# Kernel optimization log

Measured on AMD Instinct MI355X. Metric: run time of the kernel, lower is better.

The kernel has to match this reference:

```python
import jax, jax.numpy as jnp
import numpy as np
import math

MAX_LEN = 65536
NUM_HEADS = 16
HEAD_DIM = 64
K_MAX = 64
LOCAL_WINDOW = 512
LOG_N = math.ceil(math.log2(MAX_LEN + 1))   # 17
LEAF_START = 2 ** LOG_N                      # segment-tree leaf offset


def cover_set(pos):
    """O(log n) segment-tree nodes covering prefix [0..pos-1], each with leaf-depth."""
    if pos <= 0:
        return []
    l, r = LEAF_START, LEAF_START + min(pos, MAX_LEN)
    out = []
    while l < r:
        if l & 1:
            out.append((l, LOG_N - int(math.floor(math.log2(l)))))
            l += 1
        if r & 1:
            r -= 1
            out.append((r, LOG_N - int(math.floor(math.log2(r)))))
        l >>= 1
        r >>= 1
    return out


def node_content(v_tokens, node_idx, depth):
    """Content of a FULL subtree node under the concat/pairwise-mean gated merge.
    Equals: concat tokens while K<=k_max, then (left+right)/2 elementwise, which
    collapses to a strided mean over chunks of size L//K_MAX. Returns (H, K, D)."""
    L = 1 << depth
    a = (node_idx << depth) - LEAF_START          # first token covered by node
    chunk = v_tokens[a:a + L]                     # (L, H, D), static slice
    if L <= K_MAX:
        f = chunk                                 # (L, H, D)
    else:
        f = chunk.reshape(L // K_MAX, K_MAX, NUM_HEADS, HEAD_DIM).mean(0)  # (K_MAX,H,D)
    return jnp.transpose(f, (1, 0, 2))            # (H, K, D)


def setup_inputs() -> dict:
    key = jax.random.key(0)
    k1, k2, k3 = jax.random.split(key, 3)
    v_tokens = jax.random.normal(k1, (50000, NUM_HEADS, HEAD_DIM), jnp.float32)
    q_new = jax.random.normal(k2, (1, NUM_HEADS, HEAD_DIM), jnp.float32)
    depth_proj_w = jax.random.normal(k3, (LOG_N + 1, HEAD_DIM, HEAD_DIM), jnp.float32) * 0.02
    depth_temp = jnp.linspace(0.5, 4.0, LOG_N + 1).astype(jnp.float32)
    return {"v_tokens": v_tokens, "q_new": q_new, "depth_proj_w": depth_proj_w,
            "depth_temp": depth_temp, "n_tokens": 50000}


def reference(v_tokens, q_new, depth_proj_w, depth_temp, n_tokens):
    pos = int(n_tokens)
    q = q_new[0]                                   # (H, D)
    inv_sqrt_d = 1.0 / math.sqrt(HEAD_DIM)

    # --- local window attention over last min(pos, W) tokens (chronological) ---
    n_local = min(pos, LOCAL_WINDOW)
    v_local = v_tokens[pos - n_local:pos]          # (W, H, D)
    s = jnp.einsum('hd,khd->hk', q, v_local) * inv_sqrt_d
    w = jax.nn.softmax(s, axis=-1)
    local_out = jnp.einsum('hk,khd->hd', w, v_local)   # (H, D)

    # --- multi-depth causal tree attention over the O(log n) cover set ---
    node_outs = []
    for node_idx, depth in cover_set(pos):
        f = node_content(v_tokens, node_idx, depth)    # (H, K, D)
        q_depth = q + q @ depth_proj_w[depth].T        # depth-specific query delta
        scale = 1.0 / ((jax.nn.softplus(depth_temp[depth]) + 1e-6) * math.sqrt(HEAD_DIM))
        s = jnp.einsum('hd,hkd->hk', q_depth, f) * scale
        w = jnp.einsum('hk,hkd->hd', jax.nn.softmax(s, axis=-1), f)
        node_outs.append(w)
    if node_outs:
        tree_out = jnp.stack(node_outs, axis=0).mean(0)
    else:
        tree_out = jnp.zeros_like(local_out)

    return (local_out + tree_out)[None]            # (1, H, D)
```

## Files before the change

kernel.cpp:

```cpp
#include <hip/hip_runtime.h>
#include <math.h>

#define NUM_HEADS   16
#define HEAD_DIM    64
#define KMAXN       64
#define LOCAL_WIN   512
#define LOG_N       17
#define LEAF_START  131072
#define MAX_LEN_TOK 65536
#define ROW         1024
#define SLICE       65536
#define MAXN        34

typedef float vf4 __attribute__((ext_vector_type(4)));

__device__ __forceinline__ vf4 ntload(const float* p) {
    return __builtin_nontemporal_load((const vf4*)p);
}

struct K1Args {
    int nNodes;
    int a[MAXN];
    int cpb[MAXN];
    int C[MAXN];
    int CB[MAXN];
    int K[MAXN];
    int off[MAXN];
    int bbase[MAXN];
};

struct K2Args {
    int nNodes;
    int K[MAXN];
    int C[MAXN];
    int CB[MAXN];
    int off[MAXN];
    int a[MAXN];
    int depth[MAXN];
};

__global__ __launch_bounds__(256, 4) void k1_reduce(const float* __restrict__ v,
                                                    float* __restrict__ ws,
                                                    K1Args A) {
    int b = blockIdx.x;
    int node = 0;
    for (int i = 1; i < A.nNodes; ++i)
        if (b >= A.bbase[i]) node = i;
    int lb  = b - A.bbase[node];
    int K   = A.K[node];
    int kgc = (K + 3) >> 2;
    int cb  = lb / kgc;
    int kg  = lb - cb * kgc;
    int k0  = kg * 4;
    int RK  = K - k0; if (RK > 4) RK = 4;
    int c0  = cb * A.cpb[node];
    int c1  = c0 + A.cpb[node];
    int C   = A.C[node];
    if (c1 > C) c1 = C;

    int j4 = threadIdx.x * 4;

    vf4 acc0 = 0.f, acc1 = 0.f, acc2 = 0.f, acc3 = 0.f;

    if (RK == 4) {
        int c = c0;
        for (; c + 2 <= c1; c += 2) {
            const float* p0 = v + (long)(A.a[node] + c * 64 + k0) * ROW + j4;
            const float* p1 = p0 + SLICE;
            vf4 y0 = ntload(p0);
            vf4 y1 = ntload(p0 + ROW);
            vf4 y2 = ntload(p0 + 2 * ROW);
            vf4 y3 = ntload(p0 + 3 * ROW);
            vf4 z0 = ntload(p1);
            vf4 z1 = ntload(p1 + ROW);
            vf4 z2 = ntload(p1 + 2 * ROW);
            vf4 z3 = ntload(p1 + 3 * ROW);
            acc0 += y0 + z0; acc1 += y1 + z1; acc2 += y2 + z2; acc3 += y3 + z3;
        }
        if (c < c1) {
            const float* p0 = v + (long)(A.a[node] + c * 64 + k0) * ROW + j4;
            acc0 += ntload(p0);
            acc1 += ntload(p0 + ROW);
            acc2 += ntload(p0 + 2 * ROW);
            acc3 += ntload(p0 + 3 * ROW);
        }
    } else {
        for (int c = c0; c < c1; ++c) {
            const float* p0 = v + (long)(A.a[node] + c * 64 + k0) * ROW + j4;
            if (RK > 0) acc0 += ntload(p0);
            if (RK > 1) acc1 += ntload(p0 + ROW);
            if (RK > 2) acc2 += ntload(p0 + 2 * ROW);
            if (RK > 3) acc3 += ntload(p0 + 3 * ROW);
        }
    }

    float* wp = ws + (long)A.off[node] + (long)cb * SLICE + (long)k0 * ROW + j4;
    if (RK > 0) *(vf4*)(wp)           = acc0;
    if (RK > 1) *(vf4*)(wp + ROW)     = acc1;
    if (RK > 2) *(vf4*)(wp + 2 * ROW) = acc2;
    if (RK > 3) *(vf4*)(wp + 3 * ROW) = acc3;
}

__global__ __launch_bounds__(512) void k2_fused(const float* __restrict__ v,
                                                const float* __restrict__ ws,
                                                const float* __restrict__ q,
                                                const float* __restrict__ W,
                                                const float* __restrict__ temp,
                                                float* __restrict__ node_out,
                                                float* __restrict__ local_out,
                                                int pos, K2Args A) {
    int h    = blockIdx.x;
    int node = blockIdx.y;
    int tid  = threadIdx.x;
    int lane = tid & 63;
    int w    = tid >> 6;

    __shared__ float fh[64][64];
    __shared__ float qs[64], qds[64], sv[64], ps[64];
    __shared__ float red[8][64];
    __shared__ float sc[LOCAL_WIN];
    __shared__ float wred[16];
    __shared__ float mS[2];

    if (node < A.nNodes) {
        int K = A.K[node];
        if (tid < 64) qs[tid] = q[h * 64 + tid];

        const float* bp; int CB; float invC;
        if (A.C[node] > 1) {
            bp   = ws + (long)A.off[node] + h * 64;
            CB   = A.CB[node];
            invC = 1.0f / (float)A.C[node];
        } else {
            bp   = v + (long)A.a[node] * ROW + h * 64;
            CB   = 1;
            invC = 1.0f;
        }
        for (int id = tid; id < 1024; id += 512) {
            int r  = id >> 4;
            int c4 = (id & 15) << 2;
            if (r < K) {
                vf4 s0 = 0.f, s1 = 0.f, s2 = 0.f, s3 = 0.f;
                const float* p = bp + (long)r * ROW + c4;
                int cb = 0;
                for (; cb + 4 <= CB; cb += 4) {
                    s0 += *(const vf4*)(p + (long)cb * SLICE);
                    s1 += *(const vf4*)(p + (long)(cb + 1) * SLICE);
                    s2 += *(const vf4*)(p + (long)(cb + 2) * SLICE);
                    s3 += *(const vf4*)(p + (long)(cb + 3) * SLICE);
                }
                for (; cb < CB; ++cb) s0 += *(const vf4*)(p + (long)cb * SLICE);
                s0 += s1; s2 += s3; s0 += s2;
                s0 *= invC;
                *(vf4*)&fh[r][c4] = s0;
            }
        }
        __syncthreads();

        int dep = A.depth[node];
        float qp = 0.f;
        const float* Wr = W + ((long)dep * 64 + lane) * 64;
        #pragma unroll
        for (int e = w * 8; e < w * 8 + 8; ++e) qp += qs[e] * Wr[e];
        red[w][lane] = qp;
        __syncthreads();
        if (w == 0) {
            float t = qs[lane];
            #pragma unroll
            for (int i = 0; i < 8; ++i) t += red[i][lane];
            qds[lane] = t;
        }
        __syncthreads();
        float qd    = qds[lane];
        float sp    = log1pf(expf(temp[dep]));
        float scale = 1.0f / ((sp + 1e-6f) * 8.0f);

        for (int k = w; k < K; k += 8) {
            float p = qd * fh[k][lane];
            #pragma unroll
            for (int m = 1; m < 64; m <<= 1) p += __shfl_xor(p, m, 64);
            if (lane == 0) sv[k] = p * scale;
        }
        __syncthreads();

        if (w == 0) {
            float s  = (lane < K) ? sv[lane] : -1e30f;
            float mx = s;
            #pragma unroll
            for (int m = 1; m < 64; m <<= 1) mx = fmaxf(mx, __shfl_xor(mx, m, 64));
            float e = (lane < K) ? expf(s - mx) : 0.f;
            float S = e;
            #pragma unroll
            for (int m = 1; m < 64; m <<= 1) S += __shfl_xor(S, m, 64);
            ps[lane] = e / S;
        }
        __syncthreads();

        float o = 0.f;
        for (int k = w; k < K; k += 8) o += ps[k] * fh[k][lane];
        red[w][lane] = o;
        __syncthreads();
        if (w == 0) {
            float t = 0.f;
            #pragma unroll
            for (int i = 0; i < 8; ++i) t += red[i][lane];
            node_out[node * ROW + h * 64 + lane] = t;
        }
    } else {
        int nloc = pos < LOCAL_WIN ? pos : LOCAL_WIN;
        int t0   = pos - nloc;

        if (tid < 64) qs[tid] = q[h * 64 + tid];
        __syncthreads();

        float s = -1e30f;
        if (tid < nloc) {
            const float* vr = v + (long)(t0 + tid) * ROW + h * 64;
            float acc = 0.f;
            #pragma unroll 8
            for (int d = 0; d < 64; ++d) acc += qs[d] * vr[d];
            s = acc * 0.125f;
        }
        float mx = s;
        #pragma unroll
        for (int m = 1; m < 64; m <<= 1) mx = fmaxf(mx, __shfl_xor(mx, m, 64));
        if (lane == 0) wred[w] = mx;
        __syncthreads();
        if (tid == 0) {
            float m2 = wred[0];
            for (int i = 1; i < 8; ++i) m2 = fmaxf(m2, wred[i]);
            mS[0] = m2;
        }
        __syncthreads();
        float m = mS[0];

        float e = (tid < nloc) ? expf(s - m) : 0.f;
        sc[tid] = e;
        float su = e;
        #pragma unroll
        for (int mm = 1; mm < 64; mm <<= 1) su += __shfl_xor(su, mm, 64);
        if (lane == 0) wred[8 + w] = su;
        __syncthreads();
        if (tid == 0) {
            float S2 = 0.f;
            for (int i = 0; i < 8; ++i) S2 += wred[8 + i];
            mS[1] = S2;
        }
        __syncthreads();
        float S = mS[1];

        float acc = 0.f;
        {
            const float* vb = v + (long)t0 * ROW + h * 64 + lane;
            int tb = w * 64;
            #pragma unroll 4
            for (int i = 0; i < 64; ++i) {
                int t = tb + i;
                if (t < nloc) acc += sc[t] * vb[(long)t * ROW];
            }
        }
        red[w][lane] = acc;
        __syncthreads();

        if (w == 0) {
            float tot = 0.f;
            #pragma unroll
            for (int i = 0; i < 8; ++i) tot += red[i][lane];
            local_out[h * 64 + lane] = (nloc > 0) ? tot / S : 0.f;
        }
    }
}

__global__ __launch_bounds__(256) void k3_combine(const float* __restrict__ node_out,
                                                  const float* __restrict__ local_out,
                                                  int nNodes,
                                                  float* __restrict__ out) {
    int i = blockIdx.x * 256 + threadIdx.x;
    float tr = 0.f;
    for (int n = 0; n < nNodes; ++n) tr += node_out[(long)n * ROW + i];
    if (nNodes > 0) tr /= (float)nNodes;
    out[i] = local_out[i] + tr;
}

static int floor_log2_host(unsigned x) { int r = 0; while (x >>= 1) ++r; return r; }

extern "C" void kernel_launch(void* const* d_in, const int* in_sizes, int n_in,
                              void* d_out, int out_size, void* d_ws, size_t ws_size,
                              hipStream_t stream) {
    const float* v    = (const float*)d_in[0];
    const float* q    = (const float*)d_in[1];
    const float* W    = (const float*)d_in[2];
    const float* temp = (const float*)d_in[3];
    float* out        = (float*)d_out;
    float* ws         = (float*)d_ws;

    int pos = in_sizes[0] / ROW;

    int n_nodes = 0;
    int nv[MAXN], nd[MAXN];
    if (pos > 0) {
        long l = LEAF_START;
        long r = LEAF_START + (pos < MAX_LEN_TOK ? pos : MAX_LEN_TOK);
        while (l < r) {
            if (l & 1) { nv[n_nodes] = (int)l; nd[n_nodes] = LOG_N - floor_log2_host((unsigned)l); ++n_nodes; ++l; }
            if (r & 1) { --r; nv[n_nodes] = (int)r; nd[n_nodes] = LOG_N - floor_log2_host((unsigned)r); ++n_nodes; }
            l >>= 1; r >>= 1;
        }
    }

    int cpb_choice = 1024;
    for (int cand : {16, 32, 64, 128, 256, 512, 1024}) {
        long tot_cb = 0;
        for (int i = 0; i < n_nodes; ++i) {
            int L = 1 << nd[i];
            int C = (L > KMAXN) ? L / KMAXN : 1;
            if (C > 1) tot_cb += (C + cand - 1) / cand;
        }
        long need = (tot_cb * (long)SLICE + (long)n_nodes * ROW + ROW) * 4;
        if (need <= (long)ws_size) { cpb_choice = cand; break; }
    }

    K1Args A1{}; K2Args A2{};
    A2.nNodes = n_nodes;
    int off = 0, bb = 0, nBig = 0;
    for (int i = 0; i < n_nodes; ++i) {
        int depth = nd[i];
        int L = 1 << depth;
        int a = (nv[i] << depth) - LEAF_START;
        int K = (L < KMAXN) ? L : KMAXN;
        int C = (L > KMAXN) ? L / KMAXN : 1;
        A2.K[i] = K; A2.C[i] = C; A2.a[i] = a; A2.depth[i] = depth;
        if (C > 1) {
            int CB  = (C + cpb_choice - 1) / cpb_choice;
            int cpb = (C + CB - 1) / CB;
            int kgc = (K + 3) / 4;
            A1.a[nBig] = a;   A1.cpb[nBig] = cpb; A1.C[nBig] = C;
            A1.CB[nBig] = CB; A1.K[nBig] = K;
            A1.off[nBig] = off; A1.bbase[nBig] = bb;
            A2.CB[i] = CB; A2.off[i] = off;
            off += CB * SLICE;
            bb  += kgc * CB;
            ++nBig;
        } else {
            A2.CB[i] = 1; A2.off[i] = 0;
        }
    }
    A1.nNodes = nBig;

    float* node_outp  = ws + (long)off;
    float* local_outp = node_outp + (long)n_nodes * ROW;

    if (nBig > 0)
        hipLaunchKernelGGL(k1_reduce, dim3(bb), dim3(256), 0, stream, v, ws, A1);
    hipLaunchKernelGGL(k2_fused, dim3(NUM_HEADS, n_nodes + 1), dim3(512), 0, stream,
                       v, ws, q, W, temp, node_outp, local_outp, pos, A2);
    hipLaunchKernelGGL(k3_combine, dim3(4), dim3(256), 0, stream,
                       node_outp, local_outp, n_nodes, out);
}
```

Baseline: 291.8 us.

## Fuse three kernels into one cooperative persistent kernel with grid syncs

Replaces the three launches (chunk reduce, per-node attention, combine) with a single cooperative persistent kernel that uses grid-wide syncs between phases. The local-window attention is moved into the first phase so it overlaps with the chunk reduction. Block size drops to 256, and the smallest chunks-per-block candidate is removed. This is meant to cut launch overhead and inter-kernel gaps. In exchange it adds grid-sync cost, caps the grid at the number of co-resident blocks, and keeps the old three-kernel path as a fallback if the cooperative launch fails.

```diff
diff --git a/kernel.cpp b/kernel.cpp
--- a/kernel.cpp
+++ b/kernel.cpp
@@ -1,5 +1,8 @@
 #include <hip/hip_runtime.h>
+#include <hip/hip_cooperative_groups.h>
 #include <math.h>
+
+namespace cg = cooperative_groups;
 
 #define NUM_HEADS   16
 #define HEAD_DIM    64
@@ -18,25 +21,249 @@
     return __builtin_nontemporal_load((const vf4*)p);
 }
 
+struct MArgs {
+    int nBig, nNodes, pos, bbK1, nUnits, nTiles;
+    int offNodeOut, offLocalOut;
+    int a1[MAXN], cpb[MAXN], C1[MAXN], off1[MAXN], bbase[MAXN];
+    int K2n[MAXN], C2[MAXN], CB2[MAXN], off2[MAXN], a2[MAXN], dep[MAXN];
+};
+
+__global__ __launch_bounds__(256, 4) void mega(const float* __restrict__ v,
+                                               const float* __restrict__ q,
+                                               const float* __restrict__ W,
+                                               const float* __restrict__ temp,
+                                               float* __restrict__ out,
+                                               float* __restrict__ ws,
+                                               MArgs A) {
+    int tid  = threadIdx.x;
+    int lane = tid & 63;
+    int w    = tid >> 6;
+    float* node_out  = ws + A.offNodeOut;
+    float* local_out = ws + A.offLocalOut;
+
+    __shared__ float fh[64][64];
+    __shared__ float qs[64], qds[64], sv[64], ps[64];
+    __shared__ float red[4][64];
+    __shared__ float sc[LOCAL_WIN];
+    __shared__ float wred[8];
+    __shared__ float mS[2];
+
+    for (int u = blockIdx.x; u < A.nUnits; u += gridDim.x) {
+        if (u < A.bbK1) {
+            int node = 0;
+            for (int i = 1; i < A.nBig; ++i) if (u >= A.bbase[i]) node = i;
+            int lb = u - A.bbase[node];
+            int cb = lb >> 4;
+            int kg = lb & 15;
+            int k0 = kg << 2;
+            int c0 = cb * A.cpb[node];
+            int c1 = c0 + A.cpb[node];
+            if (c1 > A.C1[node]) c1 = A.C1[node];
+            int j4 = tid * 4;
+
+            vf4 acc0 = 0.f, acc1 = 0.f, acc2 = 0.f, acc3 = 0.f;
+            int c = c0;
+            for (; c + 2 <= c1; c += 2) {
+                const float* p0 = v + (long)(A.a1[node] + c * 64 + k0) * ROW + j4;
+                const float* p1 = p0 + SLICE;
+                vf4 y0 = ntload(p0);
+                vf4 y1 = ntload(p0 + ROW);
+                vf4 y2 = ntload(p0 + 2 * ROW);
+                vf4 y3 = ntload(p0 + 3 * ROW);
+                vf4 z0 = ntload(p1);
+                vf4 z1 = ntload(p1 + ROW);
+                vf4 z2 = ntload(p1 + 2 * ROW);
+                vf4 z3 = ntload(p1 + 3 * ROW);
+                acc0 += y0 + z0; acc1 += y1 + z1; acc2 += y2 + z2; acc3 += y3 + z3;
+            }
+            if (c < c1) {
+                const float* p0 = v + (long)(A.a1[node] + c * 64 + k0) * ROW + j4;
+                acc0 += ntload(p0);
+                acc1 += ntload(p0 + ROW);
+                acc2 += ntload(p0 + 2 * ROW);
+                acc3 += ntload(p0 + 3 * ROW);
+            }
+            float* wp = ws + (long)A.off1[node] + (long)cb * SLICE + (long)k0 * ROW + j4;
+            *(vf4*)(wp)           = acc0;
+            *(vf4*)(wp + ROW)     = acc1;
+            *(vf4*)(wp + 2 * ROW) = acc2;
+            *(vf4*)(wp + 3 * ROW) = acc3;
+        } else {
+            int h    = u - A.bbK1;
+            int nloc = A.pos < LOCAL_WIN ? A.pos : LOCAL_WIN;
+            int t0   = A.pos - nloc;
+
+            if (tid < 64) qs[tid] = q[h * 64 + tid];
+            __syncthreads();
+
+            float s0 = -1e30f, s1 = -1e30f;
+            if (tid < nloc) {
+                const float* vr = v + (long)(t0 + tid) * ROW + h * 64;
+                float acc = 0.f;
+                #pragma unroll 8
+                for (int d = 0; d < 64; ++d) acc += qs[d] * vr[d];
+                s0 = acc * 0.125f;
+            }
+            if (tid + 256 < nloc) {
+                const float* vr = v + (long)(t0 + tid + 256) * ROW + h * 64;
+                float acc = 0.f;
+                #pragma unroll 8
+                for (int d = 0; d < 64; ++d) acc += qs[d] * vr[d];
+                s1 = acc * 0.125f;
+            }
+            float mx = fmaxf(s0, s1);
+            #pragma unroll
+            for (int m = 1; m < 64; m <<= 1) mx = fmaxf(mx, __shfl_xor(mx, m, 64));
+            if (lane == 0) wred[w] = mx;
+            __syncthreads();
+            if (tid == 0) {
+                float m2 = wred[0];
+                for (int i = 1; i < 4; ++i) m2 = fmaxf(m2, wred[i]);
+                mS[0] = m2;
+            }
+            __syncthreads();
+            float m = mS[0];
+
+            float e0 = (tid < nloc)       ? expf(s0 - m) : 0.f;
+            float e1 = (tid + 256 < nloc) ? expf(s1 - m) : 0.f;
+            sc[tid]       = e0;
+            sc[tid + 256] = e1;
+            float su = e0 + e1;
+            #pragma unroll
+            for (int mm = 1; mm < 64; mm <<= 1) su += __shfl_xor(su, mm, 64);
+            if (lane == 0) wred[4 + w] = su;
+            __syncthreads();
+            if (tid == 0) {
+                float S2 = 0.f;
+                for (int i = 0; i < 4; ++i) S2 += wred[4 + i];
+                mS[1] = S2;
+            }
+            __syncthreads();
+            float S = mS[1];
+
+            float acc = 0.f;
+            {
+                const float* vb = v + (long)t0 * ROW + h * 64 + lane;
+                int tb = w * 128;
+                #pragma unroll 4
+                for (int i = 0; i < 128; ++i) {
+                    int t = tb + i;
+                    if (t < nloc) acc += sc[t] * vb[(long)t * ROW];
+                }
+            }
+            red[w][lane] = acc;
+            __syncthreads();
+            if (w == 0) {
+                float tot = red[0][lane] + red[1][lane] + red[2][lane] + red[3][lane];
+                local_out[h * 64 + lane] = (nloc > 0) ? tot / S : 0.f;
+            }
+            __syncthreads();
+        }
+    }
+
+    cg::this_grid().sync();
+
+    for (int t = blockIdx.x; t < A.nTiles; t += gridDim.x) {
+        int node = t >> 4;
+        int h    = t & 15;
+        int K    = A.K2n[node];
+
+        if (tid < 64) qs[tid] = q[h * 64 + tid];
+
+        const float* bp; int CB; float invC;
+        if (A.C2[node] > 1) {
+            bp   = ws + (long)A.off2[node] + h * 64;
+            CB   = A.CB2[node];
+            invC = 1.0f / (float)A.C2[node];
+        } else {
+            bp   = v + (long)A.a2[node] * ROW + h * 64;
+            CB   = 1;
+            invC = 1.0f;
+        }
+        for (int id = tid; id < 1024; id += 256) {
+            int r  = id >> 4;
+            int c4 = (id & 15) << 2;
+            if (r < K) {
+                vf4 s0 = 0.f, s1 = 0.f, s2 = 0.f, s3 = 0.f;
+                const float* p = bp + (long)r * ROW + c4;
+                int cb = 0;
+                for (; cb + 4 <= CB; cb += 4) {
+                    s0 += *(const vf4*)(p + (long)cb * SLICE);
+                    s1 += *(const vf4*)(p + (long)(cb + 1) * SLICE);
+                    s2 += *(const vf4*)(p + (long)(cb + 2) * SLICE);
+                    s3 += *(const vf4*)(p + (long)(cb + 3) * SLICE);
+                }
+                for (; cb < CB; ++cb) s0 += *(const vf4*)(p + (long)cb * SLICE);
+                s0 += s1; s2 += s3; s0 += s2;
+                s0 *= invC;
+                *(vf4*)&fh[r][c4] = s0;
+            }
+        }
+        __syncthreads();
+
+        int dep = A.dep[node];
+        float qp = 0.f;
+        const float* Wr = W + ((long)dep * 64 + lane) * 64;
+        #pragma unroll
+        for (int e = w * 16; e < w * 16 + 16; ++e) qp += qs[e] * Wr[e];
+        red[w][lane] = qp;
+        __syncthreads();
+        if (w == 0) qds[lane] = qs[lane] + red[0][lane] + red[1][lane] + red[2][lane] + red[3][lane];
+        __syncthreads();
+        float qd    = qds[lane];
+        float sp    = log1pf(expf(temp[dep]));
+        float scale = 1.0f / ((sp + 1e-6f) * 8.0f);
+
+        for (int k = w; k < K; k += 4) {
+            float p2 = qd * fh[k][lane];
+            #pragma unroll
+            for (int m = 1; m < 64; m <<= 1) p2 += __shfl_xor(p2, m, 64);
+            if (lane == 0) sv[k] = p2 * scale;
+        }
+        __syncthreads();
+
+        if (w == 0) {
+            float s  = (lane < K) ? sv[lane] : -1e30f;
+            float mx = s;
+            #pragma unroll
+            for (int m = 1; m < 64; m <<= 1) mx = fmaxf(mx, __shfl_xor(mx, m, 64));
+            float e = (lane < K) ? expf(s - mx) : 0.f;
+            float S = e;
+            #pragma unroll
+            for (int m = 1; m < 64; m <<= 1) S += __shfl_xor(S, m, 64);
+            ps[lane] = e / S;
+        }
+        __syncthreads();
+
+        float o = 0.f;
+        for (int k = w; k < K; k += 4) o += ps[k] * fh[k][lane];
+        red[w][lane] = o;
+        __syncthreads();
+        if (w == 0)
+            node_out[(long)node * ROW + h * 64 + lane] =
+                red[0][lane] + red[1][lane] + red[2][lane] + red[3][lane];
+        __syncthreads();
+    }
+
+    cg::this_grid().sync();
+
+    if (blockIdx.x < 4) {
+        int i = blockIdx.x * 256 + tid;
+        float tr = 0.f;
+        for (int n = 0; n < A.nNodes; ++n) tr += node_out[(long)n * ROW + i];
+        if (A.nNodes > 0) tr /= (float)A.nNodes;
+        out[i] = local_out[i] + tr;
+    }
+}
+
 struct K1Args {
     int nNodes;
-    int a[MAXN];
-    int cpb[MAXN];
-    int C[MAXN];
-    int CB[MAXN];
-    int K[MAXN];
-    int off[MAXN];
-    int bbase[MAXN];
+    int a[MAXN]; int cpb[MAXN]; int C[MAXN]; int CB[MAXN]; int K[MAXN];
+    int off[MAXN]; int bbase[MAXN];
 };
-
 struct K2Args {
     int nNodes;
-    int K[MAXN];
-    int C[MAXN];
-    int CB[MAXN];
-    int off[MAXN];
-    int a[MAXN];
-    int depth[MAXN];
+    int K[MAXN]; int C[MAXN]; int CB[MAXN]; int off[MAXN]; int a[MAXN]; int depth[MAXN];
 };
 
 __global__ __launch_bounds__(256, 4) void k1_reduce(const float* __restrict__ v,
@@ -57,32 +284,23 @@
     int c1  = c0 + A.cpb[node];
     int C   = A.C[node];
     if (c1 > C) c1 = C;
-
     int j4 = threadIdx.x * 4;
-
     vf4 acc0 = 0.f, acc1 = 0.f, acc2 = 0.f, acc3 = 0.f;
-
     if (RK == 4) {
         int c = c0;
         for (; c + 2 <= c1; c += 2) {
             const float* p0 = v + (long)(A.a[node] + c * 64 + k0) * ROW + j4;
             const float* p1 = p0 + SLICE;
-            vf4 y0 = ntload(p0);
-            vf4 y1 = ntload(p0 + ROW);
-            vf4 y2 = ntload(p0 + 2 * ROW);
-            vf4 y3 = ntload(p0 + 3 * ROW);
-            vf4 z0 = ntload(p1);
-            vf4 z1 = ntload(p1 + ROW);
-            vf4 z2 = ntload(p1 + 2 * ROW);
-            vf4 z3 = ntload(p1 + 3 * ROW);
+            vf4 y0 = ntload(p0); vf4 y1 = ntload(p0 + ROW);
+            vf4 y2 = ntload(p0 + 2 * ROW); vf4 y3 = ntload(p0 + 3 * ROW);
+            vf4 z0 = ntload(p1); vf4 z1 = ntload(p1 + ROW);
+            vf4 z2 = ntload(p1 + 2 * ROW); vf4 z3 = ntload(p1 + 3 * ROW);
             acc0 += y0 + z0; acc1 += y1 + z1; acc2 += y2 + z2; acc3 += y3 + z3;
         }
         if (c < c1) {
             const float* p0 = v + (long)(A.a[node] + c * 64 + k0) * ROW + j4;
-            acc0 += ntload(p0);
-            acc1 += ntload(p0 + ROW);
-            acc2 += ntload(p0 + 2 * ROW);
-            acc3 += ntload(p0 + 3 * ROW);
+            acc0 += ntload(p0); acc1 += ntload(p0 + ROW);
+            acc2 += ntload(p0 + 2 * ROW); acc3 += ntload(p0 + 3 * ROW);
         }
     } else {
         for (int c = c0; c < c1; ++c) {
@@ -93,7 +311,6 @@
             if (RK > 3) acc3 += ntload(p0 + 3 * ROW);
         }
     }
-
     float* wp = ws + (long)A.off[node] + (long)cb * SLICE + (long)k0 * ROW + j4;
     if (RK > 0) *(vf4*)(wp)           = acc0;
     if (RK > 1) *(vf4*)(wp + ROW)     = acc1;
@@ -125,20 +342,15 @@
     if (node < A.nNodes) {
         int K = A.K[node];
         if (tid < 64) qs[tid] = q[h * 64 + tid];
-
         const float* bp; int CB; float invC;
         if (A.C[node] > 1) {
-            bp   = ws + (long)A.off[node] + h * 64;
-            CB   = A.CB[node];
+            bp = ws + (long)A.off[node] + h * 64; CB = A.CB[node];
             invC = 1.0f / (float)A.C[node];
         } else {
-            bp   = v + (long)A.a[node] * ROW + h * 64;
-            CB   = 1;
-            invC = 1.0f;
+            bp = v + (long)A.a[node] * ROW + h * 64; CB = 1; invC = 1.0f;
         }
         for (int id = tid; id < 1024; id += 512) {
-            int r  = id >> 4;
-            int c4 = (id & 15) << 2;
+            int r = id >> 4; int c4 = (id & 15) << 2;
             if (r < K) {
                 vf4 s0 = 0.f, s1 = 0.f, s2 = 0.f, s3 = 0.f;
                 const float* p = bp + (long)r * ROW + c4;
@@ -150,13 +362,11 @@
                     s3 += *(const vf4*)(p + (long)(cb + 3) * SLICE);
                 }
                 for (; cb < CB; ++cb) s0 += *(const vf4*)(p + (long)cb * SLICE);
-                s0 += s1; s2 += s3; s0 += s2;
-                s0 *= invC;
+                s0 += s1; s2 += s3; s0 += s2; s0 *= invC;
                 *(vf4*)&fh[r][c4] = s0;
             }
         }
         __syncthreads();
-
         int dep = A.depth[node];
         float qp = 0.f;
         const float* Wr = W + ((long)dep * 64 + lane) * 64;
@@ -165,16 +375,15 @@
         red[w][lane] = qp;
         __syncthreads();
         if (w == 0) {
-            float t = qs[lane];
-            #pragma unroll
-            for (int i = 0; i < 8; ++i) t += red[i][lane];
-            qds[lane] = t;
-        }
-        __syncthreads();
-        float qd    = qds[lane];
-        float sp    = log1pf(expf(temp[dep]));
+            float t2 = qs[lane];
+            #pragma unroll
+            for (int i = 0; i < 8; ++i) t2 += red[i][lane];
+            qds[lane] = t2;
+        }
+        __syncthreads();
+        float qd = qds[lane];
+        float sp = log1pf(expf(temp[dep]));
         float scale = 1.0f / ((sp + 1e-6f) * 8.0f);
-
         for (int k = w; k < K; k += 8) {
             float p = qd * fh[k][lane];
             #pragma unroll
@@ -182,9 +391,8 @@
             if (lane == 0) sv[k] = p * scale;
         }
         __syncthreads();
-
         if (w == 0) {
-            float s  = (lane < K) ? sv[lane] : -1e30f;
+            float s = (lane < K) ? sv[lane] : -1e30f;
             float mx = s;
             #pragma unroll
             for (int m = 1; m < 64; m <<= 1) mx = fmaxf(mx, __shfl_xor(mx, m, 64));
@@ -195,24 +403,21 @@
             ps[lane] = e / S;
         }
         __syncthreads();
-
         float o = 0.f;
         for (int k = w; k < K; k += 8) o += ps[k] * fh[k][lane];
         red[w][lane] = o;
         __syncthreads();
         if (w == 0) {
-            float t = 0.f;
-            #pragma unroll
-            for (int i = 0; i < 8; ++i) t += red[i][lane];
-            node_out[node * ROW + h * 64 + lane] = t;
+            float t2 = 0.f;
+            #pragma unroll
+            for (int i = 0; i < 8; ++i) t2 += red[i][lane];
+            node_out[node * ROW + h * 64 + lane] = t2;
         }
     } else {
         int nloc = pos < LOCAL_WIN ? pos : LOCAL_WIN;
-        int t0   = pos - nloc;
-
+        int t0 = pos - nloc;
         if (tid < 64) qs[tid] = q[h * 64 + tid];
         __syncthreads();
-
         float s = -1e30f;
         if (tid < nloc) {
             const float* vr = v + (long)(t0 + tid) * ROW + h * 64;
@@ -233,7 +438,6 @@
         }
         __syncthreads();
         float m = mS[0];
-
         float e = (tid < nloc) ? expf(s - m) : 0.f;
         sc[tid] = e;
         float su = e;
@@ -248,7 +452,6 @@
         }
         __syncthreads();
         float S = mS[1];
-
         float acc = 0.f;
         {
             const float* vb = v + (long)t0 * ROW + h * 64 + lane;
@@ -261,7 +464,6 @@
         }
         red[w][lane] = acc;
         __syncthreads();
-
         if (w == 0) {
             float tot = 0.f;
             #pragma unroll
@@ -309,7 +511,7 @@
     }
 
     int cpb_choice = 1024;
-    for (int cand : {16, 32, 64, 128, 256, 512, 1024}) {
+    for (int cand : {32, 64, 128, 256, 512, 1024}) {
         long tot_cb = 0;
         for (int i = 0; i < n_nodes; ++i) {
             int L = 1 << nd[i];
@@ -320,7 +522,8 @@
         if (need <= (long)ws_size) { cpb_choice = cand; break; }
     }
 
-    K1Args A1{}; K2Args A2{};
+    MArgs A{}; K1Args A1{}; K2Args A2{};
+    A.nNodes = n_nodes; A.pos = pos;
     A2.nNodes = n_nodes;
     int off = 0, bb = 0, nBig = 0;
     for (int i = 0; i < n_nodes; ++i) {
@@ -329,31 +532,64 @@
         int a = (nv[i] << depth) - LEAF_START;
         int K = (L < KMAXN) ? L : KMAXN;
         int C = (L > KMAXN) ? L / KMAXN : 1;
+        A.K2n[i] = K; A.C2[i] = C; A.a2[i] = a; A.dep[i] = depth;
         A2.K[i] = K; A2.C[i] = C; A2.a[i] = a; A2.depth[i] = depth;
         if (C > 1) {
             int CB  = (C + cpb_choice - 1) / cpb_choice;
             int cpb = (C + CB - 1) / CB;
-            int kgc = (K + 3) / 4;
-            A1.a[nBig] = a;   A1.cpb[nBig] = cpb; A1.C[nBig] = C;
-            A1.CB[nBig] = CB; A1.K[nBig] = K;
-            A1.off[nBig] = off; A1.bbase[nBig] = bb;
+            A.a1[nBig] = a; A.cpb[nBig] = cpb; A.C1[nBig] = C;
+            A.off1[nBig] = off; A.bbase[nBig] = bb;
+            A1.a[nBig] = a; A1.cpb[nBig] = cpb; A1.C[nBig] = C;
+            A1.CB[nBig] = CB; A1.K[nBig] = K; A1.off[nBig] = off; A1.bbase[nBig] = bb;
+            A.CB2[i] = CB; A.off2[i] = off;
             A2.CB[i] = CB; A2.off[i] = off;
             off += CB * SLICE;
-            bb  += kgc * CB;
+            bb  += 16 * CB;
             ++nBig;
         } else {
+            A.CB2[i] = 1; A.off2[i] = 0;
             A2.CB[i] = 1; A2.off[i] = 0;
         }
     }
-    A1.nNodes = nBig;
-
-    float* node_outp  = ws + (long)off;
-    float* local_outp = node_outp + (long)n_nodes * ROW;
-
-    if (nBig > 0)
-        hipLaunchKernelGGL(k1_reduce, dim3(bb), dim3(256), 0, stream, v, ws, A1);
-    hipLaunchKernelGGL(k2_fused, dim3(NUM_HEADS, n_nodes + 1), dim3(512), 0, stream,
-                       v, ws, q, W, temp, node_outp, local_outp, pos, A2);
-    hipLaunchKernelGGL(k3_combine, dim3(4), dim3(256), 0, stream,
-                       node_outp, local_outp, n_nodes, out);
+    A.nBig = nBig; A1.nNodes = nBig;
+    A.bbK1 = bb;
+    A.nUnits = bb + NUM_HEADS;
+    A.nTiles = n_nodes * NUM_HEADS;
+    A.offNodeOut  = off;
+    A.offLocalOut = off + n_nodes * ROW;
+
+    float* node_outp  = ws + (long)A.offNodeOut;
+    float* local_outp = ws + (long)A.offLocalOut;
+
+    static int s_grid = 0;
+    if (s_grid == 0) {
+        int dev = 0;
+        hipGetDevice(&dev);
+        int perCU = 0;
+        if (hipOccupancyMaxActiveBlocksPerMultiprocessor(&perCU,
+                reinterpret_cast<const void*>(mega), 256, 0) != hipSuccess || perCU < 1)
+            perCU = 2;
+        int nCU = 0;
+        if (hipDeviceGetAttribute(&nCU, hipDeviceAttributeMultiprocessorCount, dev)
+                != hipSuccess || nCU < 1)
+            nCU = 256;
+        long g = (long)perCU * nCU;
+        if (g > 1024) g = 1024;
+        if (g < 64)   g = 64;
+        s_grid = (int)g;
+    }
+
+    void* kp[] = { (void*)&v, (void*)&q, (void*)&W, (void*)&temp,
+                   (void*)&out, (void*)&ws, (void*)&A };
+    hipError_t err = hipLaunchCooperativeKernel(
+        reinterpret_cast<const void*>(mega), dim3(s_grid), dim3(256), kp, 0, stream);
+
+    if (err != hipSuccess) {
+        if (nBig > 0)
+            hipLaunchKernelGGL(k1_reduce, dim3(bb), dim3(256), 0, stream, v, ws, A1);
+        hipLaunchKernelGGL(k2_fused, dim3(NUM_HEADS, n_nodes + 1), dim3(512), 0, stream,
+                           v, ws, q, W, temp, node_outp, local_outp, pos, A2);
+        hipLaunchKernelGGL(k3_combine, dim3(4), dim3(256), 0, stream,
+                           node_outp, local_outp, n_nodes, out);
+    }
 }
```

New measurement: 474.0 us. 62.4% more time.

## Merge reduce/local/small-node attention into one kernel; fuse combine via last-block atomic

Applied to the files above, without the earlier changes.

Restructures three launches into two. The first kernel runs the partial chunk reductions for large nodes together with local-window attention and direct attention for small nodes (C<=8). The second kernel runs attention for the large nodes, and its last block, chosen by an atomic counter, performs the final combine. This removes a launch and overlaps the small-node and local work with the bandwidth-bound reduction. Blocks drop from 512 to 256 threads, and the atomic counter path adds complexity.

```diff
diff --git a/kernel.cpp b/kernel.cpp
--- a/kernel.cpp
+++ b/kernel.cpp
@@ -18,54 +18,114 @@
     return __builtin_nontemporal_load((const vf4*)p);
 }
 
-struct K1Args {
-    int nNodes;
-    int a[MAXN];
-    int cpb[MAXN];
-    int C[MAXN];
-    int CB[MAXN];
-    int K[MAXN];
-    int off[MAXN];
-    int bbase[MAXN];
+__device__ __forceinline__ void attn_tile(const float* __restrict__ bp, int CB, float invC,
+                                          int K, int dep, int h,
+                                          const float* __restrict__ q,
+                                          const float* __restrict__ W,
+                                          const float* __restrict__ temp,
+                                          float* __restrict__ node_out_row,
+                                          float (&fh)[64][64], float* qs, float* qds,
+                                          float* sv, float* ps, float (&red)[4][64]) {
+    int tid = threadIdx.x, lane = tid & 63, w = tid >> 6;
+    if (tid < 64) qs[tid] = q[h * 64 + tid];
+    for (int id = tid; id < 1024; id += 256) {
+        int r = id >> 4, c4 = (id & 15) << 2;
+        if (r < K) {
+            vf4 s0 = 0.f, s1 = 0.f, s2 = 0.f, s3 = 0.f;
+            const float* p = bp + (long)r * ROW + c4;
+            int cb = 0;
+            for (; cb + 4 <= CB; cb += 4) {
+                s0 += *(const vf4*)(p + (long)cb * SLICE);
+                s1 += *(const vf4*)(p + (long)(cb + 1) * SLICE);
+                s2 += *(const vf4*)(p + (long)(cb + 2) * SLICE);
+                s3 += *(const vf4*)(p + (long)(cb + 3) * SLICE);
+            }
+            for (; cb < CB; ++cb) s0 += *(const vf4*)(p + (long)cb * SLICE);
+            s0 += s1; s2 += s3; s0 += s2;
+            s0 *= invC;
+            *(vf4*)&fh[r][c4] = s0;
+        }
+    }
+    __syncthreads();
+
+    float qp = 0.f;
+    const float* Wr = W + ((long)dep * 64 + lane) * 64;
+    #pragma unroll
+    for (int e = w * 16; e < w * 16 + 16; ++e) qp += qs[e] * Wr[e];
+    red[w][lane] = qp;
+    __syncthreads();
+    if (w == 0) qds[lane] = qs[lane] + red[0][lane] + red[1][lane] + red[2][lane] + red[3][lane];
+    __syncthreads();
+    float qd    = qds[lane];
+    float sp    = log1pf(expf(temp[dep]));
+    float scale = 1.0f / ((sp + 1e-6f) * 8.0f);
+
+    for (int k = w; k < K; k += 4) {
+        float p2 = qd * fh[k][lane];
+        #pragma unroll
+        for (int m = 1; m < 64; m <<= 1) p2 += __shfl_xor(p2, m, 64);
+        if (lane == 0) sv[k] = p2 * scale;
+    }
+    __syncthreads();
+
+    if (w == 0) {
+        float s  = (lane < K) ? sv[lane] : -1e30f;
+        float mx = s;
+        #pragma unroll
+        for (int m = 1; m < 64; m <<= 1) mx = fmaxf(mx, __shfl_xor(mx, m, 64));
+        float e = (lane < K) ? expf(s - mx) : 0.f;
+        float S = e;
+        #pragma unroll
+        for (int m = 1; m < 64; m <<= 1) S += __shfl_xor(S, m, 64);
+        ps[lane] = e / S;
+    }
+    __syncthreads();
+
+    float o = 0.f;
+    for (int k = w; k < K; k += 4) o += ps[k] * fh[k][lane];
+    red[w][lane] = o;
+    __syncthreads();
+    if (w == 0)
+        node_out_row[lane] = red[0][lane] + red[1][lane] + red[2][lane] + red[3][lane];
+}
+
+struct KAArgs {
+    int nPart, bbK1, nDirect, pos;
+    int offLocal, offCnt, offNodeOut;
+    int a1[MAXN], cpb1[MAXN], C1[MAXN], off1[MAXN], bbase[MAXN];
+    int aD[MAXN], CD[MAXN], KD[MAXN], depD[MAXN], idxD[MAXN];
 };
 
-struct K2Args {
-    int nNodes;
-    int K[MAXN];
-    int C[MAXN];
-    int CB[MAXN];
-    int off[MAXN];
-    int a[MAXN];
-    int depth[MAXN];
-};
-
-__global__ __launch_bounds__(256, 4) void k1_reduce(const float* __restrict__ v,
-                                                    float* __restrict__ ws,
-                                                    K1Args A) {
-    int b = blockIdx.x;
-    int node = 0;
-    for (int i = 1; i < A.nNodes; ++i)
-        if (b >= A.bbase[i]) node = i;
-    int lb  = b - A.bbase[node];
-    int K   = A.K[node];
-    int kgc = (K + 3) >> 2;
-    int cb  = lb / kgc;
-    int kg  = lb - cb * kgc;
-    int k0  = kg * 4;
-    int RK  = K - k0; if (RK > 4) RK = 4;
-    int c0  = cb * A.cpb[node];
-    int c1  = c0 + A.cpb[node];
-    int C   = A.C[node];
-    if (c1 > C) c1 = C;
-
-    int j4 = threadIdx.x * 4;
-
-    vf4 acc0 = 0.f, acc1 = 0.f, acc2 = 0.f, acc3 = 0.f;
-
-    if (RK == 4) {
+__global__ __launch_bounds__(256, 4) void kA(const float* __restrict__ v,
+                                             const float* __restrict__ q,
+                                             const float* __restrict__ W,
+                                             const float* __restrict__ temp,
+                                             float* __restrict__ ws, KAArgs A) {
+    __shared__ float fh[64][64];
+    __shared__ float qs[64], qds[64], sv[64], ps[64];
+    __shared__ float red[4][64];
+    __shared__ float sc[LOCAL_WIN];
+    __shared__ float wred[8];
+    __shared__ float mS[2];
+
+    int b = blockIdx.x, tid = threadIdx.x;
+    int lane = tid & 63, w = tid >> 6;
+    if (b == 0 && tid == 0) *((unsigned*)(ws + A.offCnt)) = 0u;
+
+    if (b < A.bbK1) {
+        int node = 0;
+        for (int i = 1; i < A.nPart; ++i) if (b >= A.bbase[i]) node = i;
+        int lb = b - A.bbase[node];
+        int cb = lb >> 4, kg = lb & 15, k0 = kg << 2;
+        int c0 = cb * A.cpb1[node];
+        int c1 = c0 + A.cpb1[node];
+        if (c1 > A.C1[node]) c1 = A.C1[node];
+        int j4 = tid * 4;
+
+        vf4 acc0 = 0.f, acc1 = 0.f, acc2 = 0.f, acc3 = 0.f;
         int c = c0;
         for (; c + 2 <= c1; c += 2) {
-            const float* p0 = v + (long)(A.a[node] + c * 64 + k0) * ROW + j4;
+            const float* p0 = v + (long)(A.a1[node] + c * 64 + k0) * ROW + j4;
             const float* p1 = p0 + SLICE;
             vf4 y0 = ntload(p0);
             vf4 y1 = ntload(p0 + ROW);
@@ -78,172 +138,65 @@
             acc0 += y0 + z0; acc1 += y1 + z1; acc2 += y2 + z2; acc3 += y3 + z3;
         }
         if (c < c1) {
-            const float* p0 = v + (long)(A.a[node] + c * 64 + k0) * ROW + j4;
+            const float* p0 = v + (long)(A.a1[node] + c * 64 + k0) * ROW + j4;
             acc0 += ntload(p0);
             acc1 += ntload(p0 + ROW);
             acc2 += ntload(p0 + 2 * ROW);
             acc3 += ntload(p0 + 3 * ROW);
         }
-    } else {
-        for (int c = c0; c < c1; ++c) {
-            const float* p0 = v + (long)(A.a[node] + c * 64 + k0) * ROW + j4;
-            if (RK > 0) acc0 += ntload(p0);
-            if (RK > 1) acc1 += ntload(p0 + ROW);
-            if (RK > 2) acc2 += ntload(p0 + 2 * ROW);
-            if (RK > 3) acc3 += ntload(p0 + 3 * ROW);
-        }
-    }
-
-    float* wp = ws + (long)A.off[node] + (long)cb * SLICE + (long)k0 * ROW + j4;
-    if (RK > 0) *(vf4*)(wp)           = acc0;
-    if (RK > 1) *(vf4*)(wp + ROW)     = acc1;
-    if (RK > 2) *(vf4*)(wp + 2 * ROW) = acc2;
-    if (RK > 3) *(vf4*)(wp + 3 * ROW) = acc3;
-}
-
-__global__ __launch_bounds__(512) void k2_fused(const float* __restrict__ v,
-                                                const float* __restrict__ ws,
-                                                const float* __restrict__ q,
-                                                const float* __restrict__ W,
-                                                const float* __restrict__ temp,
-                                                float* __restrict__ node_out,
-                                                float* __restrict__ local_out,
-                                                int pos, K2Args A) {
-    int h    = blockIdx.x;
-    int node = blockIdx.y;
-    int tid  = threadIdx.x;
-    int lane = tid & 63;
-    int w    = tid >> 6;
-
-    __shared__ float fh[64][64];
-    __shared__ float qs[64], qds[64], sv[64], ps[64];
-    __shared__ float red[8][64];
-    __shared__ float sc[LOCAL_WIN];
-    __shared__ float wred[16];
-    __shared__ float mS[2];
-
-    if (node < A.nNodes) {
-        int K = A.K[node];
+        float* wp = ws + (long)A.off1[node] + (long)cb * SLICE + (long)k0 * ROW + j4;
+        *(vf4*)(wp)           = acc0;
+        *(vf4*)(wp + ROW)     = acc1;
+        *(vf4*)(wp + 2 * ROW) = acc2;
+        *(vf4*)(wp + 3 * ROW) = acc3;
+    } else if (b < A.bbK1 + NUM_HEADS) {
+        int h    = b - A.bbK1;
+        int nloc = A.pos < LOCAL_WIN ? A.pos : LOCAL_WIN;
+        int t0   = A.pos - nloc;
+
         if (tid < 64) qs[tid] = q[h * 64 + tid];
-
-        const float* bp; int CB; float invC;
-        if (A.C[node] > 1) {
-            bp   = ws + (long)A.off[node] + h * 64;
-            CB   = A.CB[node];
-            invC = 1.0f / (float)A.C[node];
-        } else {
-            bp   = v + (long)A.a[node] * ROW + h * 64;
-            CB   = 1;
-            invC = 1.0f;
-        }
-        for (int id = tid; id < 1024; id += 512) {
-            int r  = id >> 4;
-            int c4 = (id & 15) << 2;
-            if (r < K) {
-                vf4 s0 = 0.f, s1 = 0.f, s2 = 0.f, s3 = 0.f;
-                const float* p = bp + (long)r * ROW + c4;
-                int cb = 0;
-                for (; cb + 4 <= CB; cb += 4) {
-                    s0 += *(const vf4*)(p + (long)cb * SLICE);
-                    s1 += *(const vf4*)(p + (long)(cb + 1) * SLICE);
-                    s2 += *(const vf4*)(p + (long)(cb + 2) * SLICE);
-                    s3 += *(const vf4*)(p + (long)(cb + 3) * SLICE);
-                }
-                for (; cb < CB; ++cb) s0 += *(const vf4*)(p + (long)cb * SLICE);
-                s0 += s1; s2 += s3; s0 += s2;
-                s0 *= invC;
-                *(vf4*)&fh[r][c4] = s0;
-            }
-        }
-        __syncthreads();
-
-        int dep = A.depth[node];
-        float qp = 0.f;
-        const float* Wr = W + ((long)dep * 64 + lane) * 64;
-        #pragma unroll
-        for (int e = w * 8; e < w * 8 + 8; ++e) qp += qs[e] * Wr[e];
-        red[w][lane] = qp;
-        __syncthreads();
-        if (w == 0) {
-            float t = qs[lane];
-            #pragma unroll
-            for (int i = 0; i < 8; ++i) t += red[i][lane];
-            qds[lane] = t;
-        }
-        __syncthreads();
-        float qd    = qds[lane];
-        float sp    = log1pf(expf(temp[dep]));
-        float scale = 1.0f / ((sp + 1e-6f) * 8.0f);
-
-        for (int k = w; k < K; k += 8) {
-            float p = qd * fh[k][lane];
-            #pragma unroll
-            for (int m = 1; m < 64; m <<= 1) p += __shfl_xor(p, m, 64);
-            if (lane == 0) sv[k] = p * scale;
-        }
-        __syncthreads();
-
-        if (w == 0) {
-            float s  = (lane < K) ? sv[lane] : -1e30f;
-            float mx = s;
-            #pragma unroll
-            for (int m = 1; m < 64; m <<= 1) mx = fmaxf(mx, __shfl_xor(mx, m, 64));
-            float e = (lane < K) ? expf(s - mx) : 0.f;
-            float S = e;
-            #pragma unroll
-            for (int m = 1; m < 64; m <<= 1) S += __shfl_xor(S, m, 64);
-            ps[lane] = e / S;
-        }
-        __syncthreads();
-
-        float o = 0.f;
-        for (int k = w; k < K; k += 8) o += ps[k] * fh[k][lane];
-        red[w][lane] = o;
-        __syncthreads();
-        if (w == 0) {
-            float t = 0.f;
-            #pragma unroll
-            for (int i = 0; i < 8; ++i) t += red[i][lane];
-            node_out[node * ROW + h * 64 + lane] = t;
-        }
-    } else {
-        int nloc = pos < LOCAL_WIN ? pos : LOCAL_WIN;
-        int t0   = pos - nloc;
-
-        if (tid < 64) qs[tid] = q[h * 64 + tid];
-        __syncthreads();
-
-        float s = -1e30f;
+        __syncthreads();
+
+        float s0 = -1e30f, s1 = -1e30f;
         if (tid < nloc) {
             const float* vr = v + (long)(t0 + tid) * ROW + h * 64;
             float acc = 0.f;
             #pragma unroll 8
             for (int d = 0; d < 64; ++d) acc += qs[d] * vr[d];
-            s = acc * 0.125f;
-        }
-        float mx = s;
+            s0 = acc * 0.125f;
+        }
+        if (tid + 256 < nloc) {
+            const float* vr = v + (long)(t0 + tid + 256) * ROW + h * 64;
+            float acc = 0.f;
+            #pragma unroll 8
+            for (int d = 0; d < 64; ++d) acc += qs[d] * vr[d];
+            s1 = acc * 0.125f;
+        }
+        float mx = fmaxf(s0, s1);
         #pragma unroll
         for (int m = 1; m < 64; m <<= 1) mx = fmaxf(mx, __shfl_xor(mx, m, 64));
         if (lane == 0) wred[w] = mx;
         __syncthreads();
         if (tid == 0) {
             float m2 = wred[0];
-            for (int i = 1; i < 8; ++i) m2 = fmaxf(m2, wred[i]);
+            for (int i = 1; i < 4; ++i) m2 = fmaxf(m2, wred[i]);
             mS[0] = m2;
         }
         __syncthreads();
         float m = mS[0];
 
-        float e = (tid < nloc) ? expf(s - m) : 0.f;
-        sc[tid] = e;
-        float su = e;
+        float e0 = (tid < nloc)       ? expf(s0 - m) : 0.f;
+        float e1 = (tid + 256 < nloc) ? expf(s1 - m) : 0.f;
+        sc[tid]       = e0;
+        sc[tid + 256] = e1;
+        float su = e0 + e1;
         #pragma unroll
         for (int mm = 1; mm < 64; mm <<= 1) su += __shfl_xor(su, mm, 64);
-        if (lane == 0) wred[8 + w] = su;
+        if (lane == 0) wred[4 + w] = su;
         __syncthreads();
         if (tid == 0) {
             float S2 = 0.f;
-            for (int i = 0; i < 8; ++i) S2 += wred[8 + i];
+            for (int i = 0; i < 4; ++i) S2 += wred[4 + i];
             mS[1] = S2;
         }
         __syncthreads();
@@ -252,21 +205,69 @@
         float acc = 0.f;
         {
             const float* vb = v + (long)t0 * ROW + h * 64 + lane;
-            int tb = w * 64;
+            int tb = w * 128;
             #pragma unroll 4
-            for (int i = 0; i < 64; ++i) {
+            for (int i = 0; i < 128; ++i) {
                 int t = tb + i;
                 if (t < nloc) acc += sc[t] * vb[(long)t * ROW];
             }
         }
         red[w][lane] = acc;
         __syncthreads();
-
         if (w == 0) {
-            float tot = 0.f;
-            #pragma unroll
-            for (int i = 0; i < 8; ++i) tot += red[i][lane];
-            local_out[h * 64 + lane] = (nloc > 0) ? tot / S : 0.f;
+            float tot = red[0][lane] + red[1][lane] + red[2][lane] + red[3][lane];
+            (ws + A.offLocal)[h * 64 + lane] = (nloc > 0) ? tot / S : 0.f;
+        }
+    } else {
+        int t = b - A.bbK1 - NUM_HEADS;
+        int d = t >> 4, h = t & 15;
+        attn_tile(v + (long)A.aD[d] * ROW + h * 64, A.CD[d], 1.0f / (float)A.CD[d],
+                  A.KD[d], A.depD[d], h, q, W, temp,
+                  ws + A.offNodeOut + (long)A.idxD[d] * ROW + h * 64,
+                  fh, qs, qds, sv, ps, red);
+    }
+}
+
+struct KBArgs {
+    int nPart, nNodes, nTiles;
+    int offLocal, offCnt, offNodeOut;
+    int C1[MAXN], CB1[MAXN], off1[MAXN], dep1[MAXN], idx1[MAXN];
+};
+
+__global__ __launch_bounds__(256, 4) void kB(const float* __restrict__ q,
+                                             const float* __restrict__ W,
+                                             const float* __restrict__ temp,
+                                             float* __restrict__ ws,
+                                             float* __restrict__ out, KBArgs B) {
+    __shared__ float fh[64][64];
+    __shared__ float qs[64], qds[64], sv[64], ps[64];
+    __shared__ float red[4][64];
+    __shared__ unsigned lastflag;
+
+    int t = blockIdx.x, tid = threadIdx.x;
+    int p = t >> 4, h = t & 15;
+    float* node_out = ws + B.offNodeOut;
+
+    attn_tile(ws + (long)B.off1[p] + h * 64, B.CB1[p], 1.0f / (float)B.C1[p],
+              64, B.dep1[p], h, q, W, temp,
+              node_out + (long)B.idx1[p] * ROW + h * 64,
+              fh, qs, qds, sv, ps, red);
+
+    __syncthreads();
+    if (tid == 0) {
+        __threadfence();
+        unsigned old = atomicAdd((unsigned*)(ws + B.offCnt), 1u);
+        lastflag = (old == (unsigned)(B.nTiles - 1)) ? 1u : 0u;
+    }
+    __syncthreads();
+    if (lastflag) {
+        __threadfence();
+        const float* local_out = ws + B.offLocal;
+        float invN = 1.0f / (float)B.nNodes;
+        for (int i = tid; i < ROW; i += 256) {
+            float tr = 0.f;
+            for (int n = 0; n < B.nNodes; ++n) tr += node_out[(long)n * ROW + i];
+            out[i] = local_out[i] + tr * invN;
         }
     }
 }
@@ -309,51 +310,58 @@
     }
 
     int cpb_choice = 1024;
-    for (int cand : {16, 32, 64, 128, 256, 512, 1024}) {
+    for (int cand : {32, 64, 128, 256, 512, 1024}) {
         long tot_cb = 0;
         for (int i = 0; i < n_nodes; ++i) {
             int L = 1 << nd[i];
             int C = (L > KMAXN) ? L / KMAXN : 1;
-            if (C > 1) tot_cb += (C + cand - 1) / cand;
-        }
-        long need = (tot_cb * (long)SLICE + (long)n_nodes * ROW + ROW) * 4;
+            if (C > 8) tot_cb += (C + cand - 1) / cand;
+        }
+        long need = (tot_cb * (long)SLICE + (long)n_nodes * ROW + ROW + 64) * 4;
         if (need <= (long)ws_size) { cpb_choice = cand; break; }
     }
 
-    K1Args A1{}; K2Args A2{};
-    A2.nNodes = n_nodes;
-    int off = 0, bb = 0, nBig = 0;
+    KAArgs A{}; KBArgs B{};
+    A.pos = pos;
+    B.nNodes = n_nodes;
+    int off = 0, bb = 0, nPart = 0, nDirect = 0;
     for (int i = 0; i < n_nodes; ++i) {
         int depth = nd[i];
         int L = 1 << depth;
         int a = (nv[i] << depth) - LEAF_START;
         int K = (L < KMAXN) ? L : KMAXN;
         int C = (L > KMAXN) ? L / KMAXN : 1;
-        A2.K[i] = K; A2.C[i] = C; A2.a[i] = a; A2.depth[i] = depth;
-        if (C > 1) {
+        if (C > 8) {
             int CB  = (C + cpb_choice - 1) / cpb_choice;
             int cpb = (C + CB - 1) / CB;
-            int kgc = (K + 3) / 4;
-            A1.a[nBig] = a;   A1.cpb[nBig] = cpb; A1.C[nBig] = C;
-            A1.CB[nBig] = CB; A1.K[nBig] = K;
-            A1.off[nBig] = off; A1.bbase[nBig] = bb;
-            A2.CB[i] = CB; A2.off[i] = off;
+            A.a1[nPart] = a; A.cpb1[nPart] = cpb; A.C1[nPart] = C;
+            A.off1[nPart] = off; A.bbase[nPart] = bb;
+            B.C1[nPart] = C; B.CB1[nPart] = CB; B.off1[nPart] = off;
+            B.dep1[nPart] = depth; B.idx1[nPart] = i;
             off += CB * SLICE;
-            bb  += kgc * CB;
-            ++nBig;
+            bb  += 16 * CB;
+            ++nPart;
         } else {
-            A2.CB[i] = 1; A2.off[i] = 0;
-        }
-    }
-    A1.nNodes = nBig;
-
-    float* node_outp  = ws + (long)off;
-    float* local_outp = node_outp + (long)n_nodes * ROW;
-
-    if (nBig > 0)
-        hipLaunchKernelGGL(k1_reduce, dim3(bb), dim3(256), 0, stream, v, ws, A1);
-    hipLaunchKernelGGL(k2_fused, dim3(NUM_HEADS, n_nodes + 1), dim3(512), 0, stream,
-                       v, ws, q, W, temp, node_outp, local_outp, pos, A2);
-    hipLaunchKernelGGL(k3_combine, dim3(4), dim3(256), 0, stream,
-                       node_outp, local_outp, n_nodes, out);
-}
+            A.aD[nDirect] = a; A.CD[nDirect] = C; A.KD[nDirect] = K;
+            A.depD[nDirect] = depth; A.idxD[nDirect] = i;
+            ++nDirect;
+        }
+    }
+    A.nPart = nPart; A.bbK1 = bb; A.nDirect = nDirect;
+    B.nPart = nPart; B.nTiles = nPart * NUM_HEADS;
+    A.offNodeOut = off;
+    A.offLocal   = off + n_nodes * ROW;
+    A.offCnt     = A.offLocal + ROW;
+    B.offNodeOut = A.offNodeOut; B.offLocal = A.offLocal; B.offCnt = A.offCnt;
+
+    int gridA = bb + NUM_HEADS + nDirect * NUM_HEADS;
+    hipLaunchKernelGGL(kA, dim3(gridA), dim3(256), 0, stream, v, q, W, temp, ws, A);
+
+    if (nPart > 0) {
+        hipLaunchKernelGGL(kB, dim3(B.nTiles), dim3(256), 0, stream,
+                           q, W, temp, ws, out, B);
+    } else {
+        hipLaunchKernelGGL(k3_combine, dim3(4), dim3(256), 0, stream,
+                           ws + (long)A.offNodeOut, ws + (long)A.offLocal, n_nodes, out);
+    }
+}
```

Measured after the change: 302.0 us. 1.03x slower.

## Balance chunk-block split across big nodes and fold combine into k2 via last-block counter

Applied to the files above, without the earlier changes.

Replaces the fixed chunks-per-block choice with a proportional allocation that targets about 48 partial slices in total across big nodes, shrinking the target if the workspace is too small. This changes how the k1 reduction work is spread over blocks and how many partial slices k2 must sum. It also removes the separate k3 combine launch: k2 blocks increment an atomic counter, which k1 resets, and the last block finishes the final combine. This saves one launch at the cost of a threadfence and an atomic in every k2 block, plus a serial combine inside one block.

```diff
diff --git a/kernel.cpp b/kernel.cpp
--- a/kernel.cpp
+++ b/kernel.cpp
@@ -31,6 +31,8 @@
 
 struct K2Args {
     int nNodes;
+    int nTilesTotal;
+    int doCombine;
     int K[MAXN];
     int C[MAXN];
     int CB[MAXN];
@@ -41,8 +43,10 @@
 
 __global__ __launch_bounds__(256, 4) void k1_reduce(const float* __restrict__ v,
                                                     float* __restrict__ ws,
+                                                    unsigned* __restrict__ cnt,
                                                     K1Args A) {
     int b = blockIdx.x;
+    if (b == 0 && threadIdx.x == 0) *cnt = 0u;
     int node = 0;
     for (int i = 1; i < A.nNodes; ++i)
         if (b >= A.bbase[i]) node = i;
@@ -108,6 +112,8 @@
                                                 const float* __restrict__ temp,
                                                 float* __restrict__ node_out,
                                                 float* __restrict__ local_out,
+                                                float* __restrict__ out,
+                                                unsigned* __restrict__ cnt,
                                                 int pos, K2Args A) {
     int h    = blockIdx.x;
     int node = blockIdx.y;
@@ -121,6 +127,7 @@
     __shared__ float sc[LOCAL_WIN];
     __shared__ float wred[16];
     __shared__ float mS[2];
+    __shared__ unsigned lastf;
 
     if (node < A.nNodes) {
         int K = A.K[node];
@@ -269,6 +276,27 @@
             local_out[h * 64 + lane] = (nloc > 0) ? tot / S : 0.f;
         }
     }
+
+    __threadfence();
+    __syncthreads();
+    if (tid == 0) {
+        unsigned ok = 0u;
+        if (A.doCombine) {
+            unsigned old = atomicAdd(cnt, 1u);
+            ok = (old == (unsigned)(A.nTilesTotal - 1)) ? 1u : 0u;
+        }
+        lastf = ok;
+    }
+    __syncthreads();
+    if (lastf) {
+        __threadfence();
+        float invN = 1.0f / (float)A.nNodes;
+        for (int i = tid; i < ROW; i += 512) {
+            float tr = 0.f;
+            for (int n = 0; n < A.nNodes; ++n) tr += node_out[(long)n * ROW + i];
+            out[i] = local_out[i] + tr * invN;
+        }
+    }
 }
 
 __global__ __launch_bounds__(256) void k3_combine(const float* __restrict__ node_out,
@@ -308,21 +336,51 @@
         }
     }
 
-    int cpb_choice = 1024;
-    for (int cand : {16, 32, 64, 128, 256, 512, 1024}) {
-        long tot_cb = 0;
-        for (int i = 0; i < n_nodes; ++i) {
-            int L = 1 << nd[i];
-            int C = (L > KMAXN) ? L / KMAXN : 1;
-            if (C > 1) tot_cb += (C + cand - 1) / cand;
-        }
-        long need = (tot_cb * (long)SLICE + (long)n_nodes * ROW + ROW) * 4;
-        if (need <= (long)ws_size) { cpb_choice = cand; break; }
+    int bigIdx[MAXN], bigC[MAXN], bigCB[MAXN], bigCpb[MAXN];
+    int nBig = 0; long totC = 0;
+    for (int i = 0; i < n_nodes; ++i) {
+        int L = 1 << nd[i];
+        int C = (L > KMAXN) ? L / KMAXN : 1;
+        if (C > 1) { bigIdx[nBig] = i; bigC[nBig] = C; totC += C; ++nBig; }
+    }
+    long wsFloats = (long)(ws_size / 4);
+    int TGT = 48;
+    if (nBig > 0) {
+        for (;;) {
+            long sum = 0;
+            for (int j = 0; j < nBig; ++j) {
+                int cb = (int)((long)bigC[j] * TGT / totC);
+                if (cb < 1) cb = 1;
+                if (cb > bigC[j]) cb = bigC[j];
+                bigCB[j] = cb; sum += cb;
+            }
+            while (sum < TGT) {
+                int best = -1; double br = 0.0;
+                for (int j = 0; j < nBig; ++j)
+                    if (bigCB[j] < bigC[j]) {
+                        double r2 = (double)bigC[j] / bigCB[j];
+                        if (r2 > br) { br = r2; best = j; }
+                    }
+                if (best < 0) break;
+                ++bigCB[best]; ++sum;
+            }
+            long slices = 0;
+            for (int j = 0; j < nBig; ++j) {
+                bigCpb[j] = (bigC[j] + bigCB[j] - 1) / bigCB[j];
+                bigCB[j]  = (bigC[j] + bigCpb[j] - 1) / bigCpb[j];
+                slices += bigCB[j];
+            }
+            long need = slices * (long)SLICE + (long)n_nodes * ROW + ROW + 64;
+            if (need <= wsFloats || TGT <= 8) break;
+            TGT >>= 1;
+        }
     }
 
     K1Args A1{}; K2Args A2{};
     A2.nNodes = n_nodes;
-    int off = 0, bb = 0, nBig = 0;
+    A2.nTilesTotal = NUM_HEADS * (n_nodes + 1);
+    A2.doCombine = (nBig > 0) ? 1 : 0;
+    int off = 0, bb = 0;
     for (int i = 0; i < n_nodes; ++i) {
         int depth = nd[i];
         int L = 1 << depth;
@@ -330,30 +388,29 @@
         int K = (L < KMAXN) ? L : KMAXN;
         int C = (L > KMAXN) ? L / KMAXN : 1;
         A2.K[i] = K; A2.C[i] = C; A2.a[i] = a; A2.depth[i] = depth;
-        if (C > 1) {
-            int CB  = (C + cpb_choice - 1) / cpb_choice;
-            int cpb = (C + CB - 1) / CB;
-            int kgc = (K + 3) / 4;
-            A1.a[nBig] = a;   A1.cpb[nBig] = cpb; A1.C[nBig] = C;
-            A1.CB[nBig] = CB; A1.K[nBig] = K;
-            A1.off[nBig] = off; A1.bbase[nBig] = bb;
-            A2.CB[i] = CB; A2.off[i] = off;
-            off += CB * SLICE;
-            bb  += kgc * CB;
-            ++nBig;
-        } else {
-            A2.CB[i] = 1; A2.off[i] = 0;
-        }
+        A2.CB[i] = 1; A2.off[i] = 0;
+    }
+    for (int j = 0; j < nBig; ++j) {
+        int i = bigIdx[j];
+        int K = KMAXN;
+        A1.a[j] = A2.a[i]; A1.cpb[j] = bigCpb[j]; A1.C[j] = bigC[j];
+        A1.CB[j] = bigCB[j]; A1.K[j] = K;
+        A1.off[j] = off; A1.bbase[j] = bb;
+        A2.CB[i] = bigCB[j]; A2.off[i] = off;
+        off += bigCB[j] * SLICE;
+        bb  += ((K + 3) / 4) * bigCB[j];
     }
     A1.nNodes = nBig;
 
     float* node_outp  = ws + (long)off;
     float* local_outp = node_outp + (long)n_nodes * ROW;
+    unsigned* cntp    = (unsigned*)(local_outp + ROW);
 
     if (nBig > 0)
-        hipLaunchKernelGGL(k1_reduce, dim3(bb), dim3(256), 0, stream, v, ws, A1);
+        hipLaunchKernelGGL(k1_reduce, dim3(bb), dim3(256), 0, stream, v, ws, cntp, A1);
     hipLaunchKernelGGL(k2_fused, dim3(NUM_HEADS, n_nodes + 1), dim3(512), 0, stream,
-                       v, ws, q, W, temp, node_outp, local_outp, pos, A2);
-    hipLaunchKernelGGL(k3_combine, dim3(4), dim3(256), 0, stream,
-                       node_outp, local_outp, n_nodes, out);
+                       v, ws, q, W, temp, node_outp, local_outp, out, cntp, pos, A2);
+    if (nBig == 0)
+        hipLaunchKernelGGL(k3_combine, dim3(4), dim3(256), 0, stream,
+                           node_outp, local_outp, n_nodes, out);
 }
```

Result: slower. 304.0 us (+4.2%).
